# Optimization experiments

Hardware: AMD Instinct MI355X
Metric: run time of the kernel (lower is better)

## Reference

```python
import jax, jax.numpy as jnp
import numpy as np

B, P, ENC = 64, 196, 2048
ATT, DEC, EMB = 512, 512, 512
V, MAXLEN = 10000, 30


def setup_inputs() -> dict:
    key = jax.random.key(0)
    ks = jax.random.split(key, 20)
    s = 0.02
    inp = {
        "encoder_out": jax.random.normal(ks[0], (B, P, ENC), jnp.float32),
        "captions": jax.random.randint(ks[1], (B, MAXLEN), 0, V).astype(jnp.int64),
        "caption_lengths": jax.random.randint(ks[2], (B,), 1, MAXLEN).astype(jnp.int64),
        # parameters (PyTorch Linear convention: y = x @ W.T + b)
        "emb_table": jax.random.uniform(ks[3], (V, EMB), jnp.float32, -0.1, 0.1),
        "W_enc_att": jax.random.normal(ks[4], (ATT, ENC), jnp.float32) * s,
        "b_enc_att": jnp.zeros((ATT,), jnp.float32),
        "W_dec_att": jax.random.normal(ks[5], (ATT, DEC), jnp.float32) * s,
        "b_dec_att": jnp.zeros((ATT,), jnp.float32),
        "w_full_att": jax.random.normal(ks[6], (1, ATT), jnp.float32) * s,
        "b_full_att": jnp.zeros((1,), jnp.float32),
        "W_ih": jax.random.normal(ks[7], (4 * DEC, EMB + ENC), jnp.float32) * s,
        "b_ih": jnp.zeros((4 * DEC,), jnp.float32),
        "W_hh": jax.random.normal(ks[8], (4 * DEC, DEC), jnp.float32) * s,
        "b_hh": jnp.zeros((4 * DEC,), jnp.float32),
        "W_init_h": jax.random.normal(ks[9], (DEC, ENC), jnp.float32) * s,
        "b_init_h": jnp.zeros((DEC,), jnp.float32),
        "W_init_c": jax.random.normal(ks[10], (DEC, ENC), jnp.float32) * s,
        "b_init_c": jnp.zeros((DEC,), jnp.float32),
        "W_fc": jax.random.uniform(ks[11], (V, DEC), jnp.float32, -0.1, 0.1),
        "b_fc": jnp.zeros((V,), jnp.float32),
    }
    return inp


def reference(encoder_out, captions, caption_lengths, emb_table,
              W_enc_att, b_enc_att, W_dec_att, b_dec_att,
              w_full_att, b_full_att, W_ih, b_ih, W_hh, b_hh,
              W_init_h, b_init_h, W_init_c, b_init_c, W_fc, b_fc):
    # init hidden state from mean-pooled encoder features
    mean_enc = encoder_out.mean(axis=1)                       # [B, ENC]
    h0 = mean_enc @ W_init_h.T + b_init_h                     # [B, DEC]
    c0 = mean_enc @ W_init_c.T + b_init_c                     # [B, DEC]

    # encoder-side attention projection is time-invariant: hoist out of the loop
    att1 = jnp.einsum('bpe,ae->bpa', encoder_out, W_enc_att) + b_enc_att  # [B, P, ATT]

    embeddings = emb_table[captions]                          # [B, T, EMB]
    T = captions.shape[1] - 1
    emb_steps = jnp.swapaxes(embeddings[:, :T, :], 0, 1)      # [T, B, EMB]

    def step(carry, emb_t):
        h, c = carry
        att2 = h @ W_dec_att.T + b_dec_att                    # [B, ATT]
        e = (jax.nn.relu(att1 + att2[:, None, :]) @ w_full_att.T + b_full_att)[..., 0]  # [B, P]
        alpha = jax.nn.softmax(e, axis=1)                     # [B, P]
        context = jnp.einsum('bp,bpe->be', alpha, encoder_out)  # [B, ENC]
        x = jnp.concatenate([emb_t, context], axis=1)         # [B, EMB+ENC]
        gates = x @ W_ih.T + b_ih + h @ W_hh.T + b_hh         # [B, 4*DEC]
        i, f, g, o = jnp.split(gates, 4, axis=1)
        c_new = jax.nn.sigmoid(f) * c + jax.nn.sigmoid(i) * jnp.tanh(g)
        h_new = jax.nn.sigmoid(o) * jnp.tanh(c_new)
        preds = h_new @ W_fc.T + b_fc                         # dropout in eval mode = identity
        return (h_new, c_new), (preds, alpha)

    _, (preds_seq, alpha_seq) = jax.lax.scan(step, (h0, c0), emb_steps)
    predictions = jnp.swapaxes(preds_seq, 0, 1)               # [B, T, V]
    alphas = jnp.swapaxes(alpha_seq, 0, 1)                    # [B, T, P]
    return predictions, alphas
```

## Files before the change

kernel.cpp:

```cpp
#include <hip/hip_runtime.h>
#include <cstddef>

constexpr int B_   = 64;
constexpr int P_   = 196;
constexpr int ENC_ = 2048;
constexpr int ATT_ = 512;
constexpr int DEC_ = 512;
constexpr int EMB_ = 512;
constexpr int V_   = 10000;
constexpr int MAXLEN_ = 30;
constexpr int T_   = 29;
constexpr int G4_  = 2048;
constexpr int KIH_ = 2560;
constexpr int XK2_ = 2560;

constexpr int NBLK = 256;
constexpr int TPB  = 1024;
constexpr int NT   = NBLK * TPB;
constexpr int NW   = NT / 64;
constexpr int FSTR = 16;
constexpr size_t ZS_ = (size_t)B_ * G4_;

typedef __attribute__((ext_vector_type(8))) short short8;
typedef __attribute__((ext_vector_type(4))) float f32x4;
using us = unsigned short;

__device__ __forceinline__ us f2bf(float x) {
    union { float f; unsigned u; } v; v.f = x;
    unsigned r = v.u + 0x7fff + ((v.u >> 16) & 1);
    return (us)(r >> 16);
}
__device__ __forceinline__ float bf2f(us u) {
    union { unsigned u; float f; } v; v.u = ((unsigned)u) << 16;
    return v.f;
}

__device__ __forceinline__ unsigned ld4cc(const void* p) {
    unsigned r;
    asm volatile("global_load_dword %0, %1, off sc1\n\ts_waitcnt vmcnt(0)"
                 : "=v"(r) : "v"(p) : "memory");
    return r;
}
__device__ __forceinline__ void ld4cc_x8(const float* p0, const float* p1,
                                         const float* p2, const float* p3,
                                         const float* p4, const float* p5,
                                         const float* p6, const float* p7,
                                         float* o) {
    float r0, r1, r2, r3, r4, r5, r6, r7;
    asm volatile("global_load_dword %0, %8, off sc1\n\t"
                 "global_load_dword %1, %9, off sc1\n\t"
                 "global_load_dword %2, %10, off sc1\n\t"
                 "global_load_dword %3, %11, off sc1\n\t"
                 "global_load_dword %4, %12, off sc1\n\t"
                 "global_load_dword %5, %13, off sc1\n\t"
                 "global_load_dword %6, %14, off sc1\n\t"
                 "global_load_dword %7, %15, off sc1\n\t"
                 "s_waitcnt vmcnt(0)"
                 : "=&v"(r0), "=&v"(r1), "=&v"(r2), "=&v"(r3),
                   "=&v"(r4), "=&v"(r5), "=&v"(r6), "=&v"(r7)
                 : "v"(p0), "v"(p1), "v"(p2), "v"(p3),
                   "v"(p4), "v"(p5), "v"(p6), "v"(p7) : "memory");
    o[0]=r0; o[1]=r1; o[2]=r2; o[3]=r3; o[4]=r4; o[5]=r5; o[6]=r6; o[7]=r7;
}
__device__ __forceinline__ void ld16cc_x3(const void* p0, const void* p1, const void* p2,
                                          short8* a, short8* b, short8* c) {
    short8 ra, rb, rc;
    asm volatile("global_load_dwordx4 %0, %3, off sc1\n\t"
                 "global_load_dwordx4 %1, %4, off sc1\n\t"
                 "global_load_dwordx4 %2, %5, off sc1\n\t"
                 "s_waitcnt vmcnt(0)"
                 : "=&v"(ra), "=&v"(rb), "=&v"(rc)
                 : "v"(p0), "v"(p1), "v"(p2) : "memory");
    *a = ra; *b = rb; *c = rc;
}
__device__ __forceinline__ void ld16cc_x4(const void* p0, const void* p1,
                                          const void* p2, const void* p3,
                                          short8* a, short8* b, short8* c, short8* d) {
    short8 ra, rb, rc, rd;
    asm volatile("global_load_dwordx4 %0, %4, off sc1\n\t"
                 "global_load_dwordx4 %1, %5, off sc1\n\t"
                 "global_load_dwordx4 %2, %6, off sc1\n\t"
                 "global_load_dwordx4 %3, %7, off sc1\n\t"
                 "s_waitcnt vmcnt(0)"
                 : "=&v"(ra), "=&v"(rb), "=&v"(rc), "=&v"(rd)
                 : "v"(p0), "v"(p1), "v"(p2), "v"(p3) : "memory");
    *a = ra; *b = rb; *c = rc; *d = rd;
}
__device__ __forceinline__ void ldf8cc(const void* p0, const void* p1, f32x4* a, f32x4* b) {
    f32x4 ra, rb;
    asm volatile("global_load_dwordx4 %0, %2, off sc1\n\t"
                 "global_load_dwordx4 %1, %3, off sc1\n\t"
                 "s_waitcnt vmcnt(0)"
                 : "=&v"(ra), "=&v"(rb) : "v"(p0), "v"(p1) : "memory");
    *a = ra; *b = rb;
}
__device__ __forceinline__ void st4cc(void* p, unsigned v) {
    asm volatile("global_store_dword %0, %1, off sc1" :: "v"(p), "v"(v) : "memory");
}
__device__ __forceinline__ void st2cc(void* p, unsigned v) {
    asm volatile("global_store_short %0, %1, off sc1" :: "v"(p), "v"(v) : "memory");
}
__device__ __forceinline__ float wredsum(float a) {
#pragma unroll
    for (int o = 32; o > 0; o >>= 1) a += __shfl_xor(a, o);
    return a;
}

template<bool REL>
__device__ __forceinline__ void gbar(unsigned* flags, unsigned tok) {
    asm volatile("s_waitcnt vmcnt(0)" ::: "memory");
    __syncthreads();
    if (threadIdx.x == 0)
        __hip_atomic_store(&flags[blockIdx.x * FSTR], tok,
                           REL ? __ATOMIC_RELEASE : __ATOMIC_RELAXED,
                           __HIP_MEMORY_SCOPE_AGENT);
    if (threadIdx.x < NBLK) {
        while (__hip_atomic_load(&flags[threadIdx.x * FSTR], __ATOMIC_RELAXED,
                                 __HIP_MEMORY_SCOPE_AGENT) < tok)
            __builtin_amdgcn_s_sleep(1);
    }
    __syncthreads();
}

__device__ __forceinline__ void cvt8(const float* __restrict__ src, us* __restrict__ dst) {
    const float4* p = (const float4*)src;
    float4 a = p[0], b = p[1];
    union { short8 v; us u[8]; } o;
    o.u[0] = f2bf(a.x); o.u[1] = f2bf(a.y); o.u[2] = f2bf(a.z); o.u[3] = f2bf(a.w);
    o.u[4] = f2bf(b.x); o.u[5] = f2bf(b.y); o.u[6] = f2bf(b.z); o.u[7] = f2bf(b.w);
    *(short8*)dst = o.v;
}

__device__ __forceinline__ float score8(short8 v, const f32x4& lo, const f32x4& hi,
                                        const float4& w0, const float4& w1) {
    float acc = 0.f, x;
    x = bf2f((us)v[0]) + lo[0]; acc += fmaxf(x, 0.f) * w0.x;
    x = bf2f((us)v[1]) + lo[1]; acc += fmaxf(x, 0.f) * w0.y;
    x = bf2f((us)v[2]) + lo[2]; acc += fmaxf(x, 0.f) * w0.z;
    x = bf2f((us)v[3]) + lo[3]; acc += fmaxf(x, 0.f) * w0.w;
    x = bf2f((us)v[4]) + hi[0]; acc += fmaxf(x, 0.f) * w1.x;
    x = bf2f((us)v[5]) + hi[1]; acc += fmaxf(x, 0.f) * w1.y;
    x = bf2f((us)v[6]) + hi[2]; acc += fmaxf(x, 0.f) * w1.z;
    x = bf2f((us)v[7]) + hi[3]; acc += fmaxf(x, 0.f) * w1.w;
    return acc;
}

__global__ __launch_bounds__(TPB) void k_persist(
    const float* __restrict__ enc, const int* __restrict__ captions,
    const float* __restrict__ emb_table,
    const float* __restrict__ W_enc_att, const float* __restrict__ b_enc_att,
    const float* __restrict__ W_dec_att, const float* __restrict__ b_dec_att,
    const float* __restrict__ w_full,
    const float* __restrict__ W_ih, const float* __restrict__ b_ih,
    const float* __restrict__ W_hh, const float* __restrict__ b_hh,
    const float* __restrict__ W_init_h, const float* __restrict__ b_init_h,
    const float* __restrict__ W_init_c, const float* __restrict__ b_init_c,
    const float* __restrict__ W_fc, const float* __restrict__ b_fc,
    us* encb, us* wencb, us* wdecb, us* wfcb, us* wcat2, us* wembW,
    us* winitb, us* xembA, us* att1b, us* hb, us* xcatb, us* meanbb,
    float* cst, float* att2G, float* gp, float* gpe, float* bsum,
    unsigned* flags, float* outp, float* outa)
{
    __shared__ us s_stage[64 * 520];
    __shared__ float s_e[P_];
    __shared__ float s_al[P_];
    __shared__ float s_red[32];

    const int tid = threadIdx.x, bid = blockIdx.x;
    const int gtid = bid * TPB + tid;
    const int wid  = gtid >> 6;
    const int w    = tid >> 6;
    const int lane = tid & 63;
    unsigned tok = 0;

    for (int i = gtid; i < B_*P_*ENC_/8; i += NT) cvt8(enc + (size_t)i*8, encb + (size_t)i*8);
    for (int i = gtid; i < ATT_*ENC_/8; i += NT) cvt8(W_enc_att + (size_t)i*8, wencb + (size_t)i*8);
    for (int i = gtid; i < ATT_*DEC_/8; i += NT) cvt8(W_dec_att + (size_t)i*8, wdecb + (size_t)i*8);
    for (int i = gtid; i < V_*DEC_/8;   i += NT) cvt8(W_fc + (size_t)i*8, wfcb + (size_t)i*8);
    for (int i = gtid; i < G4_*XK2_/8;  i += NT) {
        int n = (i*8) / XK2_, k = (i*8) % XK2_;
        const float* src = (k < ENC_) ? (W_ih + (size_t)n*KIH_ + EMB_ + k)
                                      : (W_hh + (size_t)n*DEC_ + (k - ENC_));
        cvt8(src, wcat2 + (size_t)i*8);
    }
    for (int i = gtid; i < G4_*EMB_/8;  i += NT)
        cvt8(W_ih + ((size_t)((i*8) / EMB_))*KIH_ + ((i*8) % EMB_), wembW + (size_t)i*8);
    for (int i = gtid; i < 1024*ENC_/8; i += NT) {
        int n = (i*8) >> 11, k = (i*8) & (ENC_ - 1);
        const float* src = (n < 512) ? (W_init_h + (size_t)n*ENC_ + k)
                                     : (W_init_c + (size_t)(n-512)*ENC_ + k);
        cvt8(src, winitb + (size_t)i*8);
    }
    for (int i = gtid; i < T_*B_*EMB_/8; i += NT) {
        int r = i >> 6, c8 = i & 63;
        int t = r >> 6, b = r & 63;
        int cap = captions[b*MAXLEN_ + t];
        cvt8(emb_table + (size_t)cap*EMB_ + c8*8, xembA + (size_t)r*EMB_ + c8*8);
    }
    if (gtid < G4_) bsum[gtid] = b_ih[gtid] + b_hh[gtid];
    if (gtid < B_*ENC_) {
        int b = gtid >> 11, e = gtid & (ENC_ - 1);
        const float* base = enc + (size_t)b*P_*ENC_ + e;
        float s = 0.f;
        for (int p = 0; p < P_; ++p) s += base[(size_t)p*ENC_];
        meanbb[gtid] = f2bf(s * (1.f / P_));
    }
    gbar<true>(flags, ++tok);

    for (int task = wid; task < 256 + 1856; task += NW) {
        const int r = lane & 15, g = lane >> 4;
        if (task < 256) {
            const int mt = task & 3, nt = task >> 2;
            const int m0 = mt*16, n0 = nt*16;
            const us* Ar = meanbb + (size_t)(m0 + r)*ENC_ + g*8;
            const us* Br = winitb + (size_t)(n0 + r)*ENC_ + g*8;
            f32x4 acc0 = {0,0,0,0}, acc1 = {0,0,0,0};
#pragma unroll 4
            for (int k0 = 0; k0 < ENC_; k0 += 64) {
                acc0 = __builtin_amdgcn_mfma_f32_16x16x32_bf16(
                    *(const short8*)(Ar + k0), *(const short8*)(Br + k0), acc0, 0, 0, 0);
                acc1 = __builtin_amdgcn_mfma_f32_16x16x32_bf16(
                    *(const short8*)(Ar + k0 + 32), *(const short8*)(Br + k0 + 32), acc1, 0, 0, 0);
            }
            const int n = n0 + r;
            if (n < 512) {
                float bv = b_init_h[n];
#pragma unroll
                for (int i = 0; i < 4; ++i) {
                    int b = m0 + g*4 + i;
                    unsigned hv = f2bf(acc0[i] + acc1[i] + bv);
                    st2cc(hb + b*DEC_ + n, hv);
                    st2cc(xcatb + (size_t)b*XK2_ + ENC_ + n, hv);
                }
            } else {
                int d = n - 512;
                float bv = b_init_c[d];
#pragma unroll
                for (int i = 0; i < 4; ++i)
                    st4cc(cst + (m0 + g*4 + i)*DEC_ + d,
                          __float_as_uint(acc0[i] + acc1[i] + bv));
            }
        } else {
            const int q = task - 256;
            const int m0 = (q >> 6) * 64, n0 = (q & 63) * 32;
            f32x4 acc[4][2] = {};
            const us* Ab = xembA + (size_t)(m0 + r)*EMB_ + g*8;
            const us* Bb = wembW + (size_t)(n0 + r)*EMB_ + g*8;
#pragma unroll 2
            for (int k0 = 0; k0 < EMB_; k0 += 32) {
                short8 af[4], bfr[2];
#pragma unroll
                for (int mi = 0; mi < 4; ++mi)
                    af[mi] = *(const short8*)(Ab + (size_t)mi*16*EMB_ + k0);
#pragma unroll
                for (int nj = 0; nj < 2; ++nj)
                    bfr[nj] = *(const short8*)(Bb + (size_t)nj*16*EMB_ + k0);
#pragma unroll
                for (int mi = 0; mi < 4; ++mi)
#pragma unroll
                    for (int nj = 0; nj < 2; ++nj)
                        acc[mi][nj] = __builtin_amdgcn_mfma_f32_16x16x32_bf16(
                            af[mi], bfr[nj], acc[mi][nj], 0, 0, 0);
            }
#pragma unroll
            for (int mi = 0; mi < 4; ++mi)
#pragma unroll
                for (int nj = 0; nj < 2; ++nj) {
                    int n = n0 + nj*16 + r;
                    float bv = bsum[n];
#pragma unroll
                    for (int i = 0; i < 4; ++i) {
                        int m = m0 + mi*16 + g*4 + i;
                        gpe[(size_t)m*G4_ + n] = acc[mi][nj][i] + bv;
                    }
                }
        }
    }
    gbar<true>(flags, ++tok);

    for (int task = wid; task < 3264; task += NW) {
        const int r = lane & 15, g = lane >> 4;
        if (task < 3136) {
            int mt = task >> 4, nt2 = task & 15;
            int m0 = mt*64, n0 = nt2*32;
            f32x4 acc[4][2] = {};
            const us* Ab = encb + (size_t)(m0 + r)*ENC_ + g*8;
            const us* Bb = wencb + (size_t)(n0 + r)*ENC_ + g*8;
#pragma unroll 2
            for (int k0 = 0; k0 < ENC_; k0 += 32) {
                short8 af[4], bfr[2];
#pragma unroll
                for (int mi = 0; mi < 4; ++mi)
                    af[mi] = *(const short8*)(Ab + (size_t)mi*16*ENC_ + k0);
#pragma unroll
                for (int nj = 0; nj < 2; ++nj)
                    bfr[nj] = *(const short8*)(Bb + (size_t)nj*16*ENC_ + k0);
#pragma unroll
                for (int mi = 0; mi < 4; ++mi)
#pragma unroll
                    for (int nj = 0; nj < 2; ++nj)
                        acc[mi][nj] = __builtin_amdgcn_mfma_f32_16x16x32_bf16(
                            af[mi], bfr[nj], acc[mi][nj], 0, 0, 0);
            }
#pragma unroll
            for (int mi = 0; mi < 4; ++mi)
#pragma unroll
                for (int nj = 0; nj < 2; ++nj) {
                    int n = n0 + nj*16 + r;
                    float bv = b_enc_att[n];
#pragma unroll
                    for (int i = 0; i < 4; ++i) {
                        int m = m0 + mi*16 + g*4 + i;
                        att1b[(size_t)m*ATT_ + n] = f2bf(acc[mi][nj][i] + bv);
                    }
                }
        } else {
            int q = task - 3136;
            int nt = q >> 2, mt = q & 3;
            const us* Ar = hb + (size_t)(mt*16 + r)*DEC_ + g*8;
            const us* Br = wdecb + (size_t)(nt*16 + r)*DEC_ + g*8;
            f32x4 acc0 = {0,0,0,0}, acc1 = {0,0,0,0};
#pragma unroll 4
            for (int k0 = 0; k0 < DEC_; k0 += 64) {
                short8 a0, a1, dum;
                ld16cc_x3(Ar + k0, Ar + k0 + 32, Ar + k0, &a0, &a1, &dum);
                acc0 = __builtin_amdgcn_mfma_f32_16x16x32_bf16(
                    a0, *(const short8*)(Br + k0), acc0, 0, 0, 0);
                acc1 = __builtin_amdgcn_mfma_f32_16x16x32_bf16(
                    a1, *(const short8*)(Br + k0 + 32), acc1, 0, 0, 0);
            }
            int n = nt*16 + r;
            float bv = b_dec_att[n];
#pragma unroll
            for (int i = 0; i < 4; ++i)
                st4cc(att2G + (size_t)(mt*16 + g*4 + i)*ATT_ + n,
                      __float_as_uint(acc0[i] + acc1[i] + bv));
        }
    }
    gbar<true>(flags, ++tok);

    for (int t = 0; t < T_; ++t) {
        {
            const int b = bid & 63, cc = bid >> 6;
            f32x4 a2lo, a2hi;
            const float* ap = att2G + (size_t)b*ATT_ + lane*8;
            ldf8cc(ap, ap + 4, &a2lo, &a2hi);
            const float4 w0 = *(const float4*)(w_full + lane*8);
            const float4 w1 = *(const float4*)(w_full + lane*8 + 4);
            const us* a1base = att1b + (size_t)b*P_*ATT_ + lane*8;
            for (int p = w; p < P_; p += 32) {
                const int p2 = p + 16;
                short8 v0 = *(const short8*)(a1base + (size_t)p*ATT_);
                short8 v1 = (p2 < P_) ? *(const short8*)(a1base + (size_t)p2*ATT_) : v0;
                float acc0 = score8(v0, a2lo, a2hi, w0, w1);
                float acc1 = score8(v1, a2lo, a2hi, w0, w1);
                acc0 = wredsum(acc0);
                acc1 = wredsum(acc1);
                if (lane == 0) {
                    s_e[p] = acc0;
                    if (p2 < P_) s_e[p2] = acc1;
                }
            }
            __syncthreads();
            float v = (tid < P_) ? s_e[tid] : -3.4e38f;
            float mx = v;
#pragma unroll
            for (int o = 32; o > 0; o >>= 1) mx = fmaxf(mx, __shfl_xor(mx, o));
            if (lane == 0) s_red[w] = mx;
            __syncthreads();
            mx = s_red[0];
#pragma unroll
            for (int j = 1; j < 16; ++j) mx = fmaxf(mx, s_red[j]);
            float ev = (tid < P_) ? expf(v - mx) : 0.f;
            float sm = wredsum(ev);
            if (lane == 0) s_red[16 + w] = sm;
            __syncthreads();
            float tot = 0.f;
#pragma unroll
            for (int j = 0; j < 16; ++j) tot += s_red[16 + j];
            if (tid < P_) {
                float al = ev / tot;
                s_al[tid] = al;
                if (cc == 0) outa[((size_t)b*T_ + t)*P_ + tid] = al;
            }
            __syncthreads();
            float a[8] = {};
            const us* ep = encb + (size_t)b*P_*ENC_ + cc*512 + lane*8;
            for (int p = w; p < P_; p += 16) {
                short8 vv = *(const short8*)(ep + (size_t)p*ENC_);
                float al = s_al[p];
#pragma unroll
                for (int j = 0; j < 8; ++j) a[j] += al * bf2f((us)vv[j]);
            }
            float* s_accf = (float*)s_stage;
            {
                f32x4 lo = {a[0],a[1],a[2],a[3]}, hi = {a[4],a[5],a[6],a[7]};
                *(f32x4*)(s_accf + w*512 + lane*8)     = lo;
                *(f32x4*)(s_accf + w*512 + lane*8 + 4) = hi;
            }
            __syncthreads();
            if (tid < 256) {
                int c2 = tid*2;
                float s0 = 0.f, s1 = 0.f;
#pragma unroll
                for (int q = 0; q < 16; ++q) {
                    s0 += s_accf[q*512 + c2];
                    s1 += s_accf[q*512 + c2 + 1];
                }
                unsigned pk = (unsigned)f2bf(s0) | ((unsigned)f2bf(s1) << 16);
                st4cc(xcatb + (size_t)b*XK2_ + cc*512 + c2, pk);
            }
            __syncthreads();
        }
        gbar<false>(flags, ++tok);

        {
            const int z = bid >> 5;
            {
                short8 v0, v1, v2;
                int c0 = tid, c1 = tid + 1024, c2i = tid + 2048;
                const us* p0 = xcatb + (size_t)(c0/40)*XK2_ + z*320 + (c0%40)*8;
                const us* p1 = xcatb + (size_t)(c1/40)*XK2_ + z*320 + (c1%40)*8;
                bool has2 = c2i < 2560;
                const us* p2 = has2 ? xcatb + (size_t)(c2i/40)*XK2_ + z*320 + (c2i%40)*8 : p0;
                ld16cc_x3(p0, p1, p2, &v0, &v1, &v2);
                *(short8*)(s_stage + (c0/40)*328 + (c0%40)*8) = v0;
                *(short8*)(s_stage + (c1/40)*328 + (c1%40)*8) = v1;
                if (has2) *(short8*)(s_stage + (c2i/40)*328 + (c2i%40)*8) = v2;
            }
            __syncthreads();
            const int nt = (bid & 31)*4 + (w >> 2), mt = w & 3;
            const int r = lane & 15, g = lane >> 4;
            const us* sxr = s_stage + (mt*16 + r)*328 + g*8;
            const us* Br  = wcat2 + (size_t)(nt*16 + r)*XK2_ + z*320 + g*8;
            f32x4 acc0 = {0,0,0,0}, acc1 = {0,0,0,0};
#pragma unroll
            for (int k0 = 0; k0 < 320; k0 += 64) {
                acc0 = __builtin_amdgcn_mfma_f32_16x16x32_bf16(
                    *(const short8*)(sxr + k0), *(const short8*)(Br + k0), acc0, 0, 0, 0);
                acc1 = __builtin_amdgcn_mfma_f32_16x16x32_bf16(
                    *(const short8*)(sxr + k0 + 32), *(const short8*)(Br + k0 + 32), acc1, 0, 0, 0);
            }
            const int n = nt*16 + r;
#pragma unroll
            for (int i = 0; i < 4; ++i) {
                int m = mt*16 + g*4 + i;
                st4cc(gp + ZS_*z + (size_t)m*G4_ + n, __float_as_uint(acc0[i] + acc1[i]));
            }
            __syncthreads();
        }
        gbar<false>(flags, ++tok);

        {
            float* sg = (float*)s_stage;
            if (tid < 512) {
                const int cell = tid & 127, gate = tid >> 7;
                const int idx = bid*128 + cell;
                const int b = idx >> 9, d = idx & 511;
                const float* gz = gp + (size_t)b*G4_ + gate*512 + d;
                float vz[8];
                ld4cc_x8(gz, gz + ZS_, gz + 2*ZS_, gz + 3*ZS_,
                         gz + 4*ZS_, gz + 5*ZS_, gz + 6*ZS_, gz + 7*ZS_, vz);
                sg[tid] = ((vz[0]+vz[1]) + (vz[2]+vz[3])) + ((vz[4]+vz[5]) + (vz[6]+vz[7]));
            }
            __syncthreads();
            if (tid < 128) {
                const int idx = bid*128 + tid;
                const int b = idx >> 9, d = idx & 511;
                const float* ge = gpe + ((size_t)(t*B_ + b))*G4_ + d;
                float gi = sg[tid]       + ge[0];
                float gf = sg[128 + tid] + ge[512];
                float gg = sg[256 + tid] + ge[1024];
                float go = sg[384 + tid] + ge[1536];
                float si = 1.f / (1.f + expf(-gi));
                float sf = 1.f / (1.f + expf(-gf));
                float so = 1.f / (1.f + expf(-go));
                float cold = __uint_as_float(ld4cc(cst + idx));
                float cn = sf * cold + si * tanhf(gg);
                float hn = so * tanhf(cn);
                st4cc(cst + idx, __float_as_uint(cn));
                unsigned hv = f2bf(hn);
                st2cc(hb + idx, hv);
                st2cc(xcatb + (size_t)b*XK2_ + ENC_ + d, hv);
            }
        }
        gbar<false>(flags, ++tok);

        if (bid < 165) {
            {
                short8 v0, v1, v2, v3;
                int c0 = tid, c1 = tid + 1024, c2i = tid + 2048, c3 = tid + 3072;
                ld16cc_x4(hb + (c0>>6)*DEC_ + (c0&63)*8, hb + (c1>>6)*DEC_ + (c1&63)*8,
                          hb + (c2i>>6)*DEC_ + (c2i&63)*8, hb + (c3>>6)*DEC_ + (c3&63)*8,
                          &v0, &v1, &v2, &v3);
                *(short8*)(s_stage + (c0>>6)*520 + (c0&63)*8) = v0;
                *(short8*)(s_stage + (c1>>6)*520 + (c1&63)*8) = v1;
                *(short8*)(s_stage + (c2i>>6)*520 + (c2i&63)*8) = v2;
                *(short8*)(s_stage + (c3>>6)*520 + (c3&63)*8) = v3;
            }
            __syncthreads();
            const int task = bid*16 + w;
            const int r = lane & 15, g = lane >> 4;
            if (task < 2628) {
                const bool pr = task < 2500;
                const int q  = pr ? task : task - 2500;
                const int nt = q >> 2, mt = q & 3;
                const us* shr = s_stage + (mt*16 + r)*520 + g*8;
                const us* Br  = (pr ? wfcb : wdecb) + (size_t)(nt*16 + r)*DEC_ + g*8;
                f32x4 acc0 = {0,0,0,0}, acc1 = {0,0,0,0};
#pragma unroll
                for (int k0 = 0; k0 < DEC_; k0 += 64) {
                    acc0 = __builtin_amdgcn_mfma_f32_16x16x32_bf16(
                        *(const short8*)(shr + k0), *(const short8*)(Br + k0), acc0, 0, 0, 0);
                    acc1 = __builtin_amdgcn_mfma_f32_16x16x32_bf16(
                        *(const short8*)(shr + k0 + 32), *(const short8*)(Br + k0 + 32), acc1, 0, 0, 0);
                }
                const int n = nt*16 + r;
                if (pr) {
                    float bv = b_fc[n];
#pragma unroll
                    for (int i = 0; i < 4; ++i) {
                        int b = mt*16 + g*4 + i;
                        outp[(size_t)b*(T_*V_) + (size_t)t*V_ + n] = acc0[i] + acc1[i] + bv;
                    }
                } else {
                    float bv = b_dec_att[n];
#pragma unroll
                    for (int i = 0; i < 4; ++i)
                        st4cc(att2G + (size_t)(mt*16 + g*4 + i)*ATT_ + n,
                              __float_as_uint(acc0[i] + acc1[i] + bv));
                }
            }
            __syncthreads();
        }
        if (t != T_ - 1) gbar<false>(flags, ++tok);
    }
}

extern "C" void kernel_launch(void* const* d_in, const int* in_sizes, int n_in,
                              void* d_out, int out_size, void* d_ws, size_t ws_size,
                              hipStream_t stream) {
    const float* enc       = (const float*)d_in[0];
    const int*   captions  = (const int*)d_in[1];
    const float* emb_table = (const float*)d_in[3];
    const float* W_enc_att = (const float*)d_in[4];
    const float* b_enc_att = (const float*)d_in[5];
    const float* W_dec_att = (const float*)d_in[6];
    const float* b_dec_att = (const float*)d_in[7];
    const float* w_full    = (const float*)d_in[8];
    const float* W_ih      = (const float*)d_in[10];
    const float* b_ih      = (const float*)d_in[11];
    const float* W_hh      = (const float*)d_in[12];
    const float* b_hh      = (const float*)d_in[13];
    const float* W_init_h  = (const float*)d_in[14];
    const float* b_init_h  = (const float*)d_in[15];
    const float* W_init_c  = (const float*)d_in[16];
    const float* b_init_c  = (const float*)d_in[17];
    const float* W_fc      = (const float*)d_in[18];
    const float* b_fc      = (const float*)d_in[19];

    char* ws = (char*)d_ws;
    size_t off = 0;
    auto alloc = [&](size_t bytes) {
        void* p = ws + off;
        off = (off + bytes + 255) & ~(size_t)255;
        return p;
    };
    us* encb   = (us*)alloc((size_t)B_ * P_ * ENC_ * 2);
    us* wencb  = (us*)alloc((size_t)ATT_ * ENC_ * 2);
    us* wdecb  = (us*)alloc((size_t)ATT_ * DEC_ * 2);
    us* wfcb   = (us*)alloc((size_t)V_ * DEC_ * 2);
    us* wcat2  = (us*)alloc((size_t)G4_ * XK2_ * 2);
    us* wembW  = (us*)alloc((size_t)G4_ * EMB_ * 2);
    us* winitb = (us*)alloc((size_t)1024 * ENC_ * 2);
    us* xembA  = (us*)alloc((size_t)T_ * B_ * EMB_ * 2);
    us* att1b  = (us*)alloc((size_t)B_ * P_ * ATT_ * 2);
    us* hb     = (us*)alloc((size_t)B_ * DEC_ * 2);
    us* xcatb  = (us*)alloc((size_t)B_ * XK2_ * 2);
    us* meanbb = (us*)alloc((size_t)B_ * ENC_ * 2);
    float* cst   = (float*)alloc((size_t)B_ * DEC_ * 4);
    float* att2G = (float*)alloc((size_t)B_ * ATT_ * 4);
    float* gp    = (float*)alloc((size_t)B_ * G4_ * 8 * 4);
    float* gpe   = (float*)alloc((size_t)T_ * B_ * G4_ * 4);
    float* bsum  = (float*)alloc((size_t)G4_ * 4);
    unsigned* flags = (unsigned*)alloc((size_t)(NBLK + 1) * FSTR * 4);

    float* outp = (float*)d_out;
    float* outa = outp + (size_t)B_ * T_ * V_;

    hipMemsetAsync(flags, 0, (NBLK + 1) * FSTR * sizeof(unsigned), stream);
    k_persist<<<NBLK, TPB, 0, stream>>>(
        enc, captions, emb_table, W_enc_att, b_enc_att, W_dec_att, b_dec_att,
        w_full, W_ih, b_ih, W_hh, b_hh, W_init_h, b_init_h, W_init_c, b_init_c,
        W_fc, b_fc,
        encb, wencb, wdecb, wfcb, wcat2, wembW, winitb, xembA, att1b, hb, xcatb,
        meanbb, cst, att2G, gp, gpe, bsum, flags, outp, outa);
}
```

Measured before the change: 1.463 ms.

## Defer vocab projection off critical path with split barrier and LDS-resident weights

Splits the per-step global barrier into arrive/wait so only 32 blocks compute the attention decoder projection on the critical path. The other blocks compute the previous step's vocabulary predictions from a double-buffered hidden state while the barrier is pending, with a tail pass after the loop for the last step. It also keeps the LSTM gate weight slice and decoder-attention weights resident in LDS, and holds the cell state in registers instead of global memory. This adds LDS pressure and more complex barrier and buffer logic.

Measured after the change: 1.204 ms. 17.7% less time.

```diff
diff --git a/kernel.cpp b/kernel.cpp
--- a/kernel.cpp
+++ b/kernel.cpp
@@ -20,6 +20,7 @@
 constexpr int NW   = NT / 64;
 constexpr int FSTR = 16;
 constexpr size_t ZS_ = (size_t)B_ * G4_;
+constexpr int NPT = 625;
 
 typedef __attribute__((ext_vector_type(8))) short short8;
 typedef __attribute__((ext_vector_type(4))) float f32x4;
@@ -107,19 +108,26 @@
 }
 
 template<bool REL>
-__device__ __forceinline__ void gbar(unsigned* flags, unsigned tok) {
+__device__ __forceinline__ void gbar_arrive(unsigned* flags, unsigned tok) {
     asm volatile("s_waitcnt vmcnt(0)" ::: "memory");
     __syncthreads();
     if (threadIdx.x == 0)
         __hip_atomic_store(&flags[blockIdx.x * FSTR], tok,
                            REL ? __ATOMIC_RELEASE : __ATOMIC_RELAXED,
                            __HIP_MEMORY_SCOPE_AGENT);
+}
+__device__ __forceinline__ void gbar_wait(unsigned* flags, unsigned tok) {
     if (threadIdx.x < NBLK) {
         while (__hip_atomic_load(&flags[threadIdx.x * FSTR], __ATOMIC_RELAXED,
                                  __HIP_MEMORY_SCOPE_AGENT) < tok)
             __builtin_amdgcn_s_sleep(1);
     }
     __syncthreads();
+}
+template<bool REL>
+__device__ __forceinline__ void gbar(unsigned* flags, unsigned tok) {
+    gbar_arrive<REL>(flags, tok);
+    gbar_wait(flags, tok);
 }
 
 __device__ __forceinline__ void cvt8(const float* __restrict__ src, us* __restrict__ dst) {
@@ -145,6 +153,37 @@
     return acc;
 }
 
+__device__ __forceinline__ void preds_task(const us* s_h, const us* __restrict__ wfcb,
+                                           const float* __restrict__ b_fc,
+                                           float* __restrict__ outp,
+                                           int nt, int tt, int lane) {
+    const int r = lane & 15, g = lane >> 4;
+    f32x4 acc[4] = {{0,0,0,0},{0,0,0,0},{0,0,0,0},{0,0,0,0}};
+    const us* Brow = wfcb + (size_t)(nt*16 + r)*DEC_ + g*8;
+    const us* As   = s_h + r*520 + g*8;
+#pragma unroll
+    for (int k0 = 0; k0 < DEC_; k0 += 64) {
+        short8 b0 = *(const short8*)(Brow + k0);
+        short8 b1 = *(const short8*)(Brow + k0 + 32);
+#pragma unroll
+        for (int mt = 0; mt < 4; ++mt) {
+            short8 a0 = *(const short8*)(As + mt*16*520 + k0);
+            short8 a1 = *(const short8*)(As + mt*16*520 + k0 + 32);
+            acc[mt] = __builtin_amdgcn_mfma_f32_16x16x32_bf16(a0, b0, acc[mt], 0, 0, 0);
+            acc[mt] = __builtin_amdgcn_mfma_f32_16x16x32_bf16(a1, b1, acc[mt], 0, 0, 0);
+        }
+    }
+    const int n = nt*16 + r;
+    const float bv = b_fc[n];
+#pragma unroll
+    for (int mt = 0; mt < 4; ++mt)
+#pragma unroll
+        for (int i = 0; i < 4; ++i) {
+            int b = mt*16 + g*4 + i;
+            outp[(size_t)b*(T_*V_) + (size_t)tt*V_ + n] = acc[mt][i] + bv;
+        }
+}
+
 __global__ __launch_bounds__(TPB) void k_persist(
     const float* __restrict__ enc, const int* __restrict__ captions,
     const float* __restrict__ emb_table,
@@ -157,11 +196,13 @@
     const float* __restrict__ W_init_c, const float* __restrict__ b_init_c,
     const float* __restrict__ W_fc, const float* __restrict__ b_fc,
     us* encb, us* wencb, us* wdecb, us* wfcb, us* wcat2, us* wembW,
-    us* winitb, us* xembA, us* att1b, us* hb, us* xcatb, us* meanbb,
+    us* winitb, us* xembA, us* att1b, us* hbuf, us* xcatb, us* meanbb,
     float* cst, float* att2G, float* gp, float* gpe, float* bsum,
     unsigned* flags, float* outp, float* outa)
 {
     __shared__ us s_stage[64 * 520];
+    __shared__ us s_wb[64 * 328];
+    __shared__ us s_wd[16 * 520];
     __shared__ float s_e[P_];
     __shared__ float s_al[P_];
     __shared__ float s_red[32];
@@ -172,6 +213,9 @@
     const int w    = tid >> 6;
     const int lane = tid & 63;
     unsigned tok = 0;
+    float creg = 0.f;
+    us* const hb0 = hbuf;
+    us* const hb1 = hbuf + (size_t)B_ * DEC_;
 
     for (int i = gtid; i < B_*P_*ENC_/8; i += NT) cvt8(enc + (size_t)i*8, encb + (size_t)i*8);
     for (int i = gtid; i < ATT_*ENC_/8; i += NT) cvt8(W_enc_att + (size_t)i*8, wencb + (size_t)i*8);
@@ -229,7 +273,7 @@
                 for (int i = 0; i < 4; ++i) {
                     int b = m0 + g*4 + i;
                     unsigned hv = f2bf(acc0[i] + acc1[i] + bv);
-                    st2cc(hb + b*DEC_ + n, hv);
+                    st2cc(hb1 + b*DEC_ + n, hv);
                     st2cc(xcatb + (size_t)b*XK2_ + ENC_ + n, hv);
                 }
             } else {
@@ -317,7 +361,7 @@
         } else {
             int q = task - 3136;
             int nt = q >> 2, mt = q & 3;
-            const us* Ar = hb + (size_t)(mt*16 + r)*DEC_ + g*8;
+            const us* Ar = hb1 + (size_t)(mt*16 + r)*DEC_ + g*8;
             const us* Br = wdecb + (size_t)(nt*16 + r)*DEC_ + g*8;
             f32x4 acc0 = {0,0,0,0}, acc1 = {0,0,0,0};
 #pragma unroll 4
@@ -338,6 +382,23 @@
         }
     }
     gbar<true>(flags, ++tok);
+
+    {
+        const int z = bid >> 5, nb = bid & 31;
+        for (int c = tid; c < 2560; c += TPB) {
+            int row = c / 40, col8 = c % 40;
+            *(short8*)(s_wb + row*328 + col8*8) =
+                *(const short8*)(wcat2 + (size_t)(nb*64 + row)*XK2_ + (size_t)z*320 + col8*8);
+        }
+        if (bid < 32)
+            for (int c = tid; c < 1024; c += TPB) {
+                int row = c >> 6, col8 = c & 63;
+                *(short8*)(s_wd + row*520 + col8*8) =
+                    *(const short8*)(wdecb + (size_t)(bid*16 + row)*DEC_ + col8*8);
+            }
+        if (tid < 128) creg = __uint_as_float(ld4cc(cst + bid*128 + tid));
+        __syncthreads();
+    }
 
     for (int t = 0; t < T_; ++t) {
         {
@@ -432,7 +493,7 @@
             const int nt = (bid & 31)*4 + (w >> 2), mt = w & 3;
             const int r = lane & 15, g = lane >> 4;
             const us* sxr = s_stage + (mt*16 + r)*328 + g*8;
-            const us* Br  = wcat2 + (size_t)(nt*16 + r)*XK2_ + z*320 + g*8;
+            const us* Br  = s_wb + ((w >> 2)*16 + r)*328 + g*8;
             f32x4 acc0 = {0,0,0,0}, acc1 = {0,0,0,0};
 #pragma unroll
             for (int k0 = 0; k0 < 320; k0 += 64) {
@@ -475,65 +536,112 @@
                 float si = 1.f / (1.f + expf(-gi));
                 float sf = 1.f / (1.f + expf(-gf));
                 float so = 1.f / (1.f + expf(-go));
-                float cold = __uint_as_float(ld4cc(cst + idx));
-                float cn = sf * cold + si * tanhf(gg);
+                float cn = sf * creg + si * tanhf(gg);
+                creg = cn;
                 float hn = so * tanhf(cn);
-                st4cc(cst + idx, __float_as_uint(cn));
                 unsigned hv = f2bf(hn);
-                st2cc(hb + idx, hv);
+                us* hnew = (t & 1) ? hb1 : hb0;
+                st2cc(hnew + idx, hv);
                 st2cc(xcatb + (size_t)b*XK2_ + ENC_ + d, hv);
             }
         }
         gbar<false>(flags, ++tok);
 
-        if (bid < 165) {
-            {
+        if (t != T_ - 1) {
+            ++tok;
+            if (bid < 32) {
+                {
+                    const us* hbn = (t & 1) ? hb1 : hb0;
+                    short8 v0, v1, v2, v3;
+                    int c0 = tid, c1 = tid + 1024, c2i = tid + 2048, c3 = tid + 3072;
+                    ld16cc_x4(hbn + (c0>>6)*DEC_ + (c0&63)*8, hbn + (c1>>6)*DEC_ + (c1&63)*8,
+                              hbn + (c2i>>6)*DEC_ + (c2i&63)*8, hbn + (c3>>6)*DEC_ + (c3&63)*8,
+                              &v0, &v1, &v2, &v3);
+                    *(short8*)(s_stage + (c0>>6)*520 + (c0&63)*8) = v0;
+                    *(short8*)(s_stage + (c1>>6)*520 + (c1&63)*8) = v1;
+                    *(short8*)(s_stage + (c2i>>6)*520 + (c2i&63)*8) = v2;
+                    *(short8*)(s_stage + (c3>>6)*520 + (c3&63)*8) = v3;
+                }
+                __syncthreads();
+                if (w < 4) {
+                    const int r = lane & 15, g = lane >> 4;
+                    const us* As = s_stage + (w*16 + r)*520 + g*8;
+                    const us* Bs = s_wd + r*520 + g*8;
+                    f32x4 acc0 = {0,0,0,0}, acc1 = {0,0,0,0};
+#pragma unroll
+                    for (int k0 = 0; k0 < DEC_; k0 += 64) {
+                        acc0 = __builtin_amdgcn_mfma_f32_16x16x32_bf16(
+                            *(const short8*)(As + k0), *(const short8*)(Bs + k0), acc0, 0, 0, 0);
+                        acc1 = __builtin_amdgcn_mfma_f32_16x16x32_bf16(
+                            *(const short8*)(As + k0 + 32), *(const short8*)(Bs + k0 + 32), acc1, 0, 0, 0);
+                    }
+                    const int n = bid*16 + r;
+                    float bv = b_dec_att[n];
+#pragma unroll
+                    for (int i = 0; i < 4; ++i)
+                        st4cc(att2G + (size_t)(w*16 + g*4 + i)*ATT_ + n,
+                              __float_as_uint(acc0[i] + acc1[i] + bv));
+                }
+                gbar_arrive<false>(flags, tok);
+                gbar_wait(flags, tok);
+            } else {
+                gbar_arrive<false>(flags, tok);
+                if (t > 0) {
+                    const us* hbo = (t & 1) ? hb0 : hb1;
+                    short8 v0, v1, v2, v3;
+                    int c0 = tid, c1 = tid + 1024, c2i = tid + 2048, c3 = tid + 3072;
+                    ld16cc_x4(hbo + (c0>>6)*DEC_ + (c0&63)*8, hbo + (c1>>6)*DEC_ + (c1&63)*8,
+                              hbo + (c2i>>6)*DEC_ + (c2i&63)*8, hbo + (c3>>6)*DEC_ + (c3&63)*8,
+                              &v0, &v1, &v2, &v3);
+                    *(short8*)(s_stage + (c0>>6)*520 + (c0&63)*8) = v0;
+                    *(short8*)(s_stage + (c1>>6)*520 + (c1&63)*8) = v1;
+                    *(short8*)(s_stage + (c2i>>6)*520 + (c2i&63)*8) = v2;
+                    *(short8*)(s_stage + (c3>>6)*520 + (c3&63)*8) = v3;
+                    __syncthreads();
+                    const int tq = (bid - 32)*3 + w;
+                    if (w < 3 && tq < NPT)
+                        preds_task(s_stage, wfcb, b_fc, outp, tq, t - 1, lane);
+                }
+                gbar_wait(flags, tok);
+            }
+        } else {
+            if (bid >= 32) {
+                const us* hbo = (t & 1) ? hb0 : hb1;
                 short8 v0, v1, v2, v3;
                 int c0 = tid, c1 = tid + 1024, c2i = tid + 2048, c3 = tid + 3072;
-                ld16cc_x4(hb + (c0>>6)*DEC_ + (c0&63)*8, hb + (c1>>6)*DEC_ + (c1&63)*8,
-                          hb + (c2i>>6)*DEC_ + (c2i&63)*8, hb + (c3>>6)*DEC_ + (c3&63)*8,
+                ld16cc_x4(hbo + (c0>>6)*DEC_ + (c0&63)*8, hbo + (c1>>6)*DEC_ + (c1&63)*8,
+                          hbo + (c2i>>6)*DEC_ + (c2i&63)*8, hbo + (c3>>6)*DEC_ + (c3&63)*8,
                           &v0, &v1, &v2, &v3);
                 *(short8*)(s_stage + (c0>>6)*520 + (c0&63)*8) = v0;
                 *(short8*)(s_stage + (c1>>6)*520 + (c1&63)*8) = v1;
                 *(short8*)(s_stage + (c2i>>6)*520 + (c2i&63)*8) = v2;
                 *(short8*)(s_stage + (c3>>6)*520 + (c3&63)*8) = v3;
-            }
-            __syncthreads();
-            const int task = bid*16 + w;
-            const int r = lane & 15, g = lane >> 4;
-            if (task < 2628) {
-                const bool pr = task < 2500;
-                const int q  = pr ? task : task - 2500;
-                const int nt = q >> 2, mt = q & 3;
-                const us* shr = s_stage + (mt*16 + r)*520 + g*8;
-                const us* Br  = (pr ? wfcb : wdecb) + (size_t)(nt*16 + r)*DEC_ + g*8;
-                f32x4 acc0 = {0,0,0,0}, acc1 = {0,0,0,0};
-#pragma unroll
-                for (int k0 = 0; k0 < DEC_; k0 += 64) {
-                    acc0 = __builtin_amdgcn_mfma_f32_16x16x32_bf16(
-                        *(const short8*)(shr + k0), *(const short8*)(Br + k0), acc0, 0, 0, 0);
-                    acc1 = __builtin_amdgcn_mfma_f32_16x16x32_bf16(
-                        *(const short8*)(shr + k0 + 32), *(const short8*)(Br + k0 + 32), acc1, 0, 0, 0);
-                }
-                const int n = nt*16 + r;
-                if (pr) {
-                    float bv = b_fc[n];
-#pragma unroll
-                    for (int i = 0; i < 4; ++i) {
-                        int b = mt*16 + g*4 + i;
-                        outp[(size_t)b*(T_*V_) + (size_t)t*V_ + n] = acc0[i] + acc1[i] + bv;
-                    }
-                } else {
-                    float bv = b_dec_att[n];
-#pragma unroll
-                    for (int i = 0; i < 4; ++i)
-                        st4cc(att2G + (size_t)(mt*16 + g*4 + i)*ATT_ + n,
-                              __float_as_uint(acc0[i] + acc1[i] + bv));
-                }
-            }
-            __syncthreads();
-        }
-        if (t != T_ - 1) gbar<false>(flags, ++tok);
+                __syncthreads();
+                const int tq = (bid - 32)*3 + w;
+                if (w < 3 && tq < NPT)
+                    preds_task(s_stage, wfcb, b_fc, outp, tq, t - 1, lane);
+            }
+        }
+    }
+
+    if (bid < 40) {
+        __syncthreads();
+        const us* hbn = ((T_ - 1) & 1) ? hb1 : hb0;
+        {
+            short8 v0, v1, v2, v3;
+            int c0 = tid, c1 = tid + 1024, c2i = tid + 2048, c3 = tid + 3072;
+            ld16cc_x4(hbn + (c0>>6)*DEC_ + (c0&63)*8, hbn + (c1>>6)*DEC_ + (c1&63)*8,
+                      hbn + (c2i>>6)*DEC_ + (c2i&63)*8, hbn + (c3>>6)*DEC_ + (c3&63)*8,
+                      &v0, &v1, &v2, &v3);
+            *(short8*)(s_stage + (c0>>6)*520 + (c0&63)*8) = v0;
+            *(short8*)(s_stage + (c1>>6)*520 + (c1&63)*8) = v1;
+            *(short8*)(s_stage + (c2i>>6)*520 + (c2i&63)*8) = v2;
+            *(short8*)(s_stage + (c3>>6)*520 + (c3&63)*8) = v3;
+        }
+        __syncthreads();
+        const int tq = bid*16 + w;
+        if (tq < NPT)
+            preds_task(s_stage, wfcb, b_fc, outp, tq, T_ - 1, lane);
     }
 }
 
@@ -575,7 +683,7 @@
     us* winitb = (us*)alloc((size_t)1024 * ENC_ * 2);
     us* xembA  = (us*)alloc((size_t)T_ * B_ * EMB_ * 2);
     us* att1b  = (us*)alloc((size_t)B_ * P_ * ATT_ * 2);
-    us* hb     = (us*)alloc((size_t)B_ * DEC_ * 2);
+    us* hbuf   = (us*)alloc((size_t)2 * B_ * DEC_ * 2);
     us* xcatb  = (us*)alloc((size_t)B_ * XK2_ * 2);
     us* meanbb = (us*)alloc((size_t)B_ * ENC_ * 2);
     float* cst   = (float*)alloc((size_t)B_ * DEC_ * 4);
@@ -593,6 +701,6 @@
         enc, captions, emb_table, W_enc_att, b_enc_att, W_dec_att, b_dec_att,
         w_full, W_ih, b_ih, W_hh, b_hh, W_init_h, b_init_h, W_init_c, b_init_c,
         W_fc, b_fc,
-        encb, wencb, wdecb, wfcb, wcat2, wembW, winitb, xembA, att1b, hb, xcatb,
+        encb, wencb, wdecb, wfcb, wcat2, wembW, winitb, xembA, att1b, hbuf, xcatb,
         meanbb, cst, att2G, gp, gpe, bsum, flags, outp, outa);
 }
```
